# Kernel tuning notes

Measured on AMD Instinct MI355X. Metric: run time of the kernel, lower is better.

The kernel has to match this reference:

```python
import jax, jax.numpy as jnp
import numpy as np

B, N, D, S, ITERS = 64, 4096, 256, 8, 3
EPS = 1e-5


def _ln(x, g, b):
    m = jnp.mean(x, axis=-1, keepdims=True)
    v = jnp.mean((x - m) ** 2, axis=-1, keepdims=True)
    return (x - m) * jax.lax.rsqrt(v + EPS) * g + b


def setup_inputs() -> dict:
    key = jax.random.key(0)
    ks = jax.random.split(key, 20)
    s = 1.0 / np.sqrt(D)
    inp = {
        'x': jax.random.normal(ks[0], (B, N, D), jnp.float32),
        'noise': jax.random.normal(ks[1], (B, S, D), jnp.float32),
        'slot_mu': jax.random.normal(ks[2], (1, 1, D), jnp.float32),
        'slot_sigma': jax.random.normal(ks[3], (1, 1, D), jnp.float32) * 0.1,
        'Wq': jax.random.uniform(ks[4], (D, D), jnp.float32, -s, s),
        'bq': jnp.zeros((D,), jnp.float32),
        'Wk': jax.random.uniform(ks[5], (D, D), jnp.float32, -s, s),
        'bk': jnp.zeros((D,), jnp.float32),
        'Wv': jax.random.uniform(ks[6], (D, D), jnp.float32, -s, s),
        'bv': jnp.zeros((D,), jnp.float32),
        'W_ih': jax.random.uniform(ks[7], (3 * D, D), jnp.float32, -s, s),
        'b_ih': jnp.zeros((3 * D,), jnp.float32),
        'W_hh': jax.random.uniform(ks[8], (3 * D, D), jnp.float32, -s, s),
        'b_hh': jnp.zeros((3 * D,), jnp.float32),
        'W1': jax.random.uniform(ks[9], (D, D), jnp.float32, -s, s),
        'b1': jnp.zeros((D,), jnp.float32),
        'W2': jax.random.uniform(ks[10], (D, D), jnp.float32, -s, s),
        'b2': jnp.zeros((D,), jnp.float32),
        'g_in': jnp.ones((D,), jnp.float32), 'be_in': jnp.zeros((D,), jnp.float32),
        'g_sl': jnp.ones((D,), jnp.float32), 'be_sl': jnp.zeros((D,), jnp.float32),
        'g_mlp': jnp.ones((D,), jnp.float32), 'be_mlp': jnp.zeros((D,), jnp.float32),
    }
    return inp


def reference(x, noise, slot_mu, slot_sigma, Wq, bq, Wk, bk, Wv, bv,
              W_ih, b_ih, W_hh, b_hh, W1, b1, W2, b2,
              g_in, be_in, g_sl, be_sl, g_mlp, be_mlp):
    # slot init: mu + exp(sigma) * noise, broadcast over (B, S, D)
    slots = slot_mu + jnp.exp(slot_sigma) * noise

    xn = _ln(x, g_in, be_in)
    k = jnp.einsum('bnd,ed->bne', xn, Wk) + bk
    v = jnp.einsum('bnd,ed->bne', xn, Wv) + bv

    for _ in range(ITERS):
        sn = _ln(slots, g_sl, be_sl)
        q = jnp.einsum('bsd,ed->bse', sn, Wq) + bq
        attn_logits = jnp.einsum('bsd,bnd->bsn', q, k)
        attn = jax.nn.softmax(attn_logits, axis=-1)  # softmax over inputs N (as in source)
        updates = jnp.einsum('bnd,bsn->bsd', v, attn)

        # GRUCell: input=updates, hidden=slots (flattened over B*S)
        u = updates.reshape(-1, D)
        h = slots.reshape(-1, D)
        gx = u @ W_ih.T + b_ih
        gh = h @ W_hh.T + b_hh
        xr, xz, xn_g = jnp.split(gx, 3, axis=-1)
        hr, hz, hn_g = jnp.split(gh, 3, axis=-1)
        r = jax.nn.sigmoid(xr + hr)
        z = jax.nn.sigmoid(xz + hz)
        n = jnp.tanh(xn_g + r * hn_g)
        h = (1.0 - z) * n + z * h
        slots = h.reshape(x.shape[0], -1, D)

        m = _ln(slots, g_mlp, be_mlp)
        slots = slots + jax.nn.relu(m @ W1.T + b1) @ W2.T + b2
    return slots
```

## Files before the change

kernel.cpp:

```cpp
#include <hip/hip_runtime.h>

#define B_ 64
#define N_ 4096
#define D_ 256
#define S_ 8
#define EPSL 1e-5f

typedef _Float16 f16x8 __attribute__((ext_vector_type(8)));
typedef _Float16 f16x4 __attribute__((ext_vector_type(4)));
typedef float f32x4 __attribute__((ext_vector_type(4)));

__device__ __forceinline__ void gload_lds16(const void* g, void* l){
    __builtin_amdgcn_global_load_lds(
        (const __attribute__((address_space(1))) unsigned int*)g,
        (__attribute__((address_space(3))) unsigned int*)l, 16, 0, 0);
}

__global__ __launch_bounds__(256) void k_ln_x(const float* __restrict__ x,
        const float* __restrict__ g, const float* __restrict__ be,
        _Float16* __restrict__ xn) {
    int w = threadIdx.x >> 6, l = threadIdx.x & 63;
    long row = (long)blockIdx.x * 4 + w;
    float4 xv = *(const float4*)(x + row * D_ + l * 4);
    float s = xv.x + xv.y + xv.z + xv.w;
    float q = xv.x*xv.x + xv.y*xv.y + xv.z*xv.z + xv.w*xv.w;
    #pragma unroll
    for (int m = 1; m < 64; m <<= 1) { s += __shfl_xor(s, m); q += __shfl_xor(q, m); }
    float mean = s * (1.0f/D_);
    float var = q * (1.0f/D_) - mean*mean;
    float inv = rsqrtf(var + EPSL);
    float4 gv = *(const float4*)(g + l*4);
    float4 bv = *(const float4*)(be + l*4);
    f16x4 o;
    o[0] = (_Float16)((xv.x-mean)*inv*gv.x + bv.x);
    o[1] = (_Float16)((xv.y-mean)*inv*gv.y + bv.y);
    o[2] = (_Float16)((xv.z-mean)*inv*gv.z + bv.z);
    o[3] = (_Float16)((xv.w-mean)*inv*gv.w + bv.w);
    *(f16x4*)(xn + row * D_ + l*4) = o;
}

__global__ __launch_bounds__(256) void k_wprep(const float* __restrict__ Whh,
        const float* __restrict__ W1, const float* __restrict__ W2,
        _Float16* __restrict__ Whhf, _Float16* __restrict__ W1f,
        _Float16* __restrict__ W2f) {
    int r = blockIdx.x, t = threadIdx.x;
    const float* src; _Float16* dst; int row;
    if (r < 768){ src = Whh; dst = Whhf; row = r; }
    else if (r < 1024){ src = W1; dst = W1f; row = r - 768; }
    else { src = W2; dst = W2f; row = r - 1024; }
    float v = src[(long)(r < 768 ? r : (r < 1024 ? r-768 : r-1024))*256 + t];
    long di = (long)((((row>>4)*8 + (t>>5))*64 + ((t>>3)&3)*16 + (row&15)))*8 + (t&7);
    dst[di] = (_Float16)v;
}

__global__ __launch_bounds__(256) void k_wprep2(const float* __restrict__ Wih,
        const float* __restrict__ Wv, const float* __restrict__ Wq,
        const float* __restrict__ Wk, const float* __restrict__ bih,
        const float* __restrict__ bv, const float* __restrict__ bq,
        _Float16* __restrict__ Wcf, _Float16* __restrict__ Wqkf,
        float* __restrict__ bc, float* __restrict__ cq) {
    __shared__ float a[4][256];
    int r = blockIdx.x, t = threadIdx.x;
    int w = t>>6, l = t&63;
    bool isC = (r < 192);
    if (isC){
        #pragma unroll
        for (int k=0;k<4;k++) a[k][t] = Wih[(long)(r*4+k)*256 + t];
    } else {
        int dbase = (r-192)*4;
        #pragma unroll
        for (int k=0;k<4;k++) a[k][t] = Wk[(long)t*256 + dbase + k];
    }
    __syncthreads();
    float ac[4] = {0.f,0.f,0.f,0.f};
    const float* Bm = isC ? Wv : Wq;
    for (int e=0;e<256;e++){
        float bvv = Bm[(long)e*256 + t];
        ac[0] += a[0][e]*bvv; ac[1] += a[1][e]*bvv;
        ac[2] += a[2][e]*bvv; ac[3] += a[3][e]*bvv;
    }
    _Float16* dst = isC ? Wcf : Wqkf;
    int rb = isC ? r*4 : (r-192)*4;
    #pragma unroll
    for (int k=0;k<4;k++){
        int row = rb + k;
        long di = (long)((((row>>4)*8 + (t>>5))*64 + ((t>>3)&3)*16 + (row&15)))*8 + (t&7);
        dst[di] = (_Float16)ac[k];
    }
    if (w < 4){
        const float* bvec = isC ? bv : bq;
        float p = 0.f;
        #pragma unroll
        for (int q=0;q<4;q++) p += a[w][l + q*64] * bvec[l + q*64];
        #pragma unroll
        for (int m=1;m<64;m<<=1) p += __shfl_xor(p, m);
        if (l==0){
            if (isC) bc[r*4 + w] = p + bih[r*4 + w];
            else     cq[(r-192)*4 + w] = p;
        }
    }
}

__device__ __forceinline__ void a16_st4(_Float16* a, int row, int col, float4 v){
    int byte = row*512 + ((col*2) ^ ((row&7)<<4));
    f16x4 h; h[0]=(_Float16)v.x; h[1]=(_Float16)v.y; h[2]=(_Float16)v.z; h[3]=(_Float16)v.w;
    *(f16x4*)((char*)a + byte) = h;
}
__device__ __forceinline__ void a16_st2(_Float16* a, int row, int col, _Float16 v){
    int byte = row*512 + ((col*2) ^ ((row&7)<<4));
    *(_Float16*)((char*)a + byte) = v;
}
__device__ __forceinline__ f16x8 a16_ld8(const _Float16* a, int row, int col){
    int byte = row*512 + ((col*2) ^ ((row&7)<<4));
    return *(const f16x8*)((const char*)a + byte);
}
__device__ __forceinline__ f16x8 wfrag_ld(const _Float16* __restrict__ Wf,
        int tt, int ks, int l){
    return *(const f16x8*)(Wf + ((long)tt*4096 + (ks*64 + l)*8));
}

template<int NT, int OS>
__device__ __forceinline__ void mm_stage_f(const _Float16* a16,
        const _Float16* __restrict__ Wf, float* outl, int w, int l){
    int lr = l&15, lh = l>>4;
    f16x8 A[8];
    #pragma unroll
    for (int ks=0;ks<8;ks++) A[ks] = a16_ld8(a16, lr, lh*8 + ks*32);
    #pragma unroll
    for (int tile=0; tile<NT; ++tile){
        int tt = w*NT + tile;
        f32x4 acc = {0.f,0.f,0.f,0.f};
        #pragma unroll
        for (int ks=0;ks<8;ks++)
            acc = __builtin_amdgcn_mfma_f32_16x16x32_f16(A[ks], wfrag_ld(Wf,tt,ks,l), acc, 0,0,0);
        if (lh < 2){
            #pragma unroll
            for (int r=0;r<4;r++) outl[(lh*4+r)*OS + tt*16 + lr] = acc[r];
        }
    }
}

__device__ __forceinline__ void mm_gates_f(const _Float16* au, const _Float16* ah,
        const _Float16* __restrict__ Wcf, const _Float16* __restrict__ Whf,
        float* g1, float* g2, int w, int l){
    int lr = l&15, lh = l>>4;
    f16x8 Au[8], Ah[8];
    #pragma unroll
    for (int ks=0;ks<8;ks++){ Au[ks] = a16_ld8(au, lr, lh*8+ks*32);
                              Ah[ks] = a16_ld8(ah, lr, lh*8+ks*32); }
    #pragma unroll
    for (int tile=0; tile<6; ++tile){
        int tt = w*6 + tile;
        f32x4 a1 = {0.f,0.f,0.f,0.f}, a2 = {0.f,0.f,0.f,0.f};
        #pragma unroll
        for (int ks=0;ks<8;ks++)
            a1 = __builtin_amdgcn_mfma_f32_16x16x32_f16(Au[ks], wfrag_ld(Wcf,tt,ks,l), a1, 0,0,0);
        #pragma unroll
        for (int ks=0;ks<8;ks++)
            a2 = __builtin_amdgcn_mfma_f32_16x16x32_f16(Ah[ks], wfrag_ld(Whf,tt,ks,l), a2, 0,0,0);
        if (lh < 2){
            #pragma unroll
            for (int r=0;r<4;r++){
                int s = lh*4+r;
                g1[s*768 + tt*16 + lr] = a1[r];
                g2[s*768 + tt*16 + lr] = a2[r];
            }
        }
    }
}

__global__ __launch_bounds__(512) void k_init(const float* __restrict__ noise,
        const float* __restrict__ mu, const float* __restrict__ sg,
        const float* __restrict__ g_sl, const float* __restrict__ be_sl,
        const _Float16* __restrict__ Wqkf, const float* __restrict__ cq,
        float* __restrict__ slots, _Float16* __restrict__ qh16) {
    __shared__ __align__(16) _Float16 a16[16*256];
    __shared__ float g1[8*256];
    int t = threadIdx.x, w = t>>6, l = t&63, b = blockIdx.x;
    int col = l*4;
    float4 nz = *(const float4*)(noise + ((long)b*8+w)*256 + col);
    float4 muv = *(const float4*)(mu + col);
    float4 sgv = *(const float4*)(sg + col);
    float4 sl;
    sl.x = muv.x + __expf(sgv.x)*nz.x; sl.y = muv.y + __expf(sgv.y)*nz.y;
    sl.z = muv.z + __expf(sgv.z)*nz.z; sl.w = muv.w + __expf(sgv.w)*nz.w;
    *(float4*)(slots + ((long)b*8+w)*256 + col) = sl;
    float s1 = sl.x+sl.y+sl.z+sl.w;
    float s2 = sl.x*sl.x+sl.y*sl.y+sl.z*sl.z+sl.w*sl.w;
    #pragma unroll
    for (int m=1;m<64;m<<=1){ s1+=__shfl_xor(s1,m); s2+=__shfl_xor(s2,m); }
    float mean = s1*(1.0f/D_);
    float inv = rsqrtf(s2*(1.0f/D_) - mean*mean + EPSL);
    float4 gv = *(const float4*)(g_sl + col);
    float4 bb = *(const float4*)(be_sl + col);
    float4 sn;
    sn.x=(sl.x-mean)*inv*gv.x+bb.x; sn.y=(sl.y-mean)*inv*gv.y+bb.y;
    sn.z=(sl.z-mean)*inv*gv.z+bb.z; sn.w=(sl.w-mean)*inv*gv.w+bb.w;
    a16_st4(a16, w, col, sn);
    float4 z = {0.f,0.f,0.f,0.f};
    a16_st4(a16, 8+w, col, z);
    __syncthreads();
    mm_stage_f<2,256>(a16, Wqkf, g1, w, l);
    __syncthreads();
    for (int idx=t; idx<2048; idx+=512){
        int s = idx>>8, d = idx&255;
        qh16[((long)b*16+s)*D_ + d] = (_Float16)(g1[s*256+d] + cq[d]);
        qh16[((long)b*16+8+s)*D_ + d] = (_Float16)0.f;
    }
}

__global__ __launch_bounds__(256) void k_attn(const _Float16* __restrict__ xn,
        const _Float16* __restrict__ qh16,
        float* __restrict__ pacc, float* __restrict__ ppsum,
        float* __restrict__ pmax) {
    __shared__ __align__(16) char xt_raw[4*16384];
    __shared__ __align__(16) float pt_s[4][16][8];
    __shared__ float mw_s[4][8], psw_s[4][8];
    int t = threadIdx.x, w = t>>6, l = t&63, lr = l&15, lh = l>>4;
    int c = blockIdx.x, b = blockIdx.y;

    f16x8 A[8];
    const _Float16* qbase = qh16 + ((long)b*16 + lr)*D_ + lh*8;
    #pragma unroll
    for (int ks=0;ks<8;ks++) A[ks] = *(const f16x8*)(qbase + ks*32);
    asm volatile("s_waitcnt vmcnt(0)" ::: "memory");

    char* xw = xt_raw + w*16384;
    const char* xnb = (const char*)(xn + (long)b*N_*D_);
    int rlo = l>>5;
    int cb  = (l&31)*16;

    {
        int n0 = c*512 + w*16;
        #pragma unroll
        for (int j=0;j<8;j++){
            int row = 2*j + rlo;
            const char* gp = xnb + (long)(n0+row)*512 + (cb ^ ((row&7)<<4));
            gload_lds16(gp, xw + j*1024);
        }
    }

    float m8[8];
    #pragma unroll
    for (int s=0;s<8;s++) m8[s] = -1e30f;
    float acc[8][4] = {};
    float psr[4] = {0.f,0.f,0.f,0.f};
    float (*pt)[8] = pt_s[w];
    int fx = (lr&7)<<4;

    for (int sc=0; sc<8; ++sc){
        const char* curb = xw + ((sc&1)<<13);
        char* nxtb = xw + (((sc+1)&1)<<13);
        if (sc < 7){
            asm volatile("s_waitcnt lgkmcnt(0)" ::: "memory");
            int n0n = c*512 + (sc+1)*64 + w*16;
            #pragma unroll
            for (int j=0;j<8;j++){
                int row = 2*j + rlo;
                const char* gp = xnb + (long)(n0n+row)*512 + (cb ^ ((row&7)<<4));
                gload_lds16(gp, nxtb + j*1024);
            }
            asm volatile("s_waitcnt vmcnt(8)" ::: "memory");
        } else {
            asm volatile("s_waitcnt vmcnt(0)" ::: "memory");
        }
        __builtin_amdgcn_sched_barrier(0);

        f32x4 lacc = {0.f,0.f,0.f,0.f};
        #pragma unroll
        for (int ks=0;ks<8;ks++){
            f16x8 Bf = *(const f16x8*)(curb + lr*512 + ((lh*16 + ks*64) ^ fx));
            lacc = __builtin_amdgcn_mfma_f32_16x16x32_f16(A[ks], Bf, lacc, 0,0,0);
        }
        float tm[4];
        #pragma unroll
        for (int r=0;r<4;r++) tm[r] = lacc[r];
        #pragma unroll
        for (int m=1;m<16;m<<=1){
            #pragma unroll
            for (int r=0;r<4;r++) tm[r] = fmaxf(tm[r], __shfl_xor(tm[r], m));
        }
        float mN[8];
        #pragma unroll
        for (int r=0;r<4;r++){ mN[r] = __shfl(tm[r], lr); mN[4+r] = __shfl(tm[r], 16+lr); }
        float sc8[8];
        #pragma unroll
        for (int s=0;s<8;s++){
            float mn = fmaxf(m8[s], mN[s]);
            sc8[s] = __expf(m8[s] - mn);
            m8[s] = mn;
        }
        #pragma unroll
        for (int s=0;s<8;s++){
            acc[s][0]*=sc8[s]; acc[s][1]*=sc8[s]; acc[s][2]*=sc8[s]; acc[s][3]*=sc8[s];
        }
        if (lh < 2){
            float4 pv;
            #pragma unroll
            for (int r=0;r<4;r++){
                int s = lh*4+r;
                float p = __expf(lacc[r] - m8[s]);
                psr[r] = psr[r]*sc8[s] + p;
                ((float*)&pv)[r] = p;
            }
            *(float4*)&pt[lr][lh*4] = pv;
        }
        #pragma unroll 4
        for (int i=0;i<16;i++){
            float4 p0 = *(const float4*)&pt[i][0];
            float4 p1 = *(const float4*)&pt[i][4];
            f16x4 xv = *(const f16x4*)(curb + i*512 + ((l*8) ^ ((i&7)<<4)));
            float x0=(float)xv[0], x1=(float)xv[1], x2=(float)xv[2], x3=(float)xv[3];
            acc[0][0]+=p0.x*x0; acc[0][1]+=p0.x*x1; acc[0][2]+=p0.x*x2; acc[0][3]+=p0.x*x3;
            acc[1][0]+=p0.y*x0; acc[1][1]+=p0.y*x1; acc[1][2]+=p0.y*x2; acc[1][3]+=p0.y*x3;
            acc[2][0]+=p0.z*x0; acc[2][1]+=p0.z*x1; acc[2][2]+=p0.z*x2; acc[2][3]+=p0.z*x3;
            acc[3][0]+=p0.w*x0; acc[3][1]+=p0.w*x1; acc[3][2]+=p0.w*x2; acc[3][3]+=p0.w*x3;
            acc[4][0]+=p1.x*x0; acc[4][1]+=p1.x*x1; acc[4][2]+=p1.x*x2; acc[4][3]+=p1.x*x3;
            acc[5][0]+=p1.y*x0; acc[5][1]+=p1.y*x1; acc[5][2]+=p1.y*x2; acc[5][3]+=p1.y*x3;
            acc[6][0]+=p1.z*x0; acc[6][1]+=p1.z*x1; acc[6][2]+=p1.z*x2; acc[6][3]+=p1.z*x3;
            acc[7][0]+=p1.w*x0; acc[7][1]+=p1.w*x1; acc[7][2]+=p1.w*x2; acc[7][3]+=p1.w*x3;
        }
    }
    #pragma unroll
    for (int m=1;m<16;m<<=1){
        #pragma unroll
        for (int r=0;r<4;r++) psr[r] += __shfl_xor(psr[r], m);
    }
    if (l == 0){
        #pragma unroll
        for (int s=0;s<8;s++) mw_s[w][s] = m8[s];
        #pragma unroll
        for (int r=0;r<4;r++) psw_s[w][r] = psr[r];
    }
    if (l == 16){
        #pragma unroll
        for (int r=0;r<4;r++) psw_s[w][4+r] = psr[r];
    }
    __syncthreads();
    float M8[8];
    #pragma unroll
    for (int s=0;s<8;s++)
        M8[s] = fmaxf(fmaxf(mw_s[0][s],mw_s[1][s]), fmaxf(mw_s[2][s],mw_s[3][s]));
    float* accw = (float*)xt_raw;
    #pragma unroll
    for (int s=0;s<8;s++){
        float wsc = __expf(m8[s] - M8[s]);
        float4 v;
        v.x=acc[s][0]*wsc; v.y=acc[s][1]*wsc; v.z=acc[s][2]*wsc; v.w=acc[s][3]*wsc;
        *(float4*)&accw[((w*8+s)<<8) + l*4] = v;
    }
    __syncthreads();
    for (int pair=t; pair<2048; pair+=256){
        int s = pair>>8, d = pair&255;
        float v = accw[(s<<8)+d] + accw[((8+s)<<8)+d] + accw[((16+s)<<8)+d] + accw[((24+s)<<8)+d];
        pacc[(((long)b*8 + c)*8 + s)*D_ + d] = v;
    }
    if (t < 8){
        float ps = 0.f;
        #pragma unroll
        for (int w2=0;w2<4;w2++) ps += __expf(mw_s[w2][t]-M8[t]) * psw_s[w2][t];
        ppsum[((long)b*8+c)*8 + t] = ps;
        pmax [((long)b*8+c)*8 + t] = M8[t];
    }
}

__global__ __launch_bounds__(512) void k_tail(
    const float* __restrict__ pacc, const float* __restrict__ ppsum,
    const float* __restrict__ pmax, const float* __restrict__ slots,
    const _Float16* __restrict__ Wcf, const float* __restrict__ bc,
    const _Float16* __restrict__ Whhf, const float* __restrict__ bhh,
    const _Float16* __restrict__ W1f, const float* __restrict__ b1,
    const _Float16* __restrict__ W2f, const float* __restrict__ b2,
    const float* __restrict__ gm, const float* __restrict__ bem,
    const float* __restrict__ g_sl, const float* __restrict__ be_sl,
    const _Float16* __restrict__ Wqkf, const float* __restrict__ cq,
    float* __restrict__ out, _Float16* __restrict__ qh16, int last) {
    int t = threadIdx.x, w = t>>6, l = t&63;
    int b = blockIdx.x;
    __shared__ float hb[8][256], hn[8][256];
    __shared__ float g1[8*768], g2[8*768];
    __shared__ __align__(16) _Float16 a16a[16*256], a16b[16*256];
    __shared__ float pss[8];
    __shared__ float wcs[8][8];

    if (t < 8){
        float pm[8]; float M = -1e30f;
        #pragma unroll
        for (int c=0;c<8;c++){ pm[c] = pmax[((long)b*8+c)*8+t]; M = fmaxf(M, pm[c]); }
        float ps = 0.f;
        #pragma unroll
        for (int c=0;c<8;c++){
            float wc = __expf(pm[c]-M);
            wcs[t][c] = wc;
            ps += wc*ppsum[((long)b*8+c)*8+t];
        }
        pss[t] = ps;
    }
    __syncthreads();
    for (int idx=t; idx<2048; idx+=512){
        int s = idx>>8, d = idx&255;
        float v = 0.f;
        #pragma unroll
        for (int c=0;c<8;c++) v += wcs[s][c]*pacc[(((long)b*8+c)*8+s)*D_ + d];
        float axv = v / pss[s];
        float hbv = slots[((long)b*8+s)*D_ + d];
        hb[s][d] = hbv;
        a16_st2(a16a, s, d, (_Float16)axv);
        a16_st2(a16b, s, d, (_Float16)hbv);
    }
    {   float4 z = {0.f,0.f,0.f,0.f};
        a16_st4(a16a, 8+w, l*4, z);
        a16_st4(a16b, 8+w, l*4, z);
    }
    __syncthreads();
    mm_gates_f(a16a, a16b, Wcf, Whhf, g1, g2, w, l);
    __syncthreads();
    {
        int d0 = l*4;
        float hn4[4];
        #pragma unroll
        for (int i=0;i<4;i++){
            int d = d0+i;
            float r = 1.f/(1.f+__expf(-(g1[w*768+d]     + bc[d]     + g2[w*768+d]     + bhh[d])));
            float z = 1.f/(1.f+__expf(-(g1[w*768+256+d] + bc[256+d] + g2[w*768+256+d] + bhh[256+d])));
            float gg = g1[w*768+512+d] + bc[512+d] + r*(g2[w*768+512+d] + bhh[512+d]);
            float e2 = __expf(2.f*gg);
            float nn = 1.f - 2.f/(e2+1.f);
            hn4[i] = (1.f-z)*nn + z*hb[w][d];
            hn[w][d] = hn4[i];
        }
        float s1 = hn4[0]+hn4[1]+hn4[2]+hn4[3];
        float s2 = hn4[0]*hn4[0]+hn4[1]*hn4[1]+hn4[2]*hn4[2]+hn4[3]*hn4[3];
        #pragma unroll
        for (int m=1;m<64;m<<=1){ s1+=__shfl_xor(s1,m); s2+=__shfl_xor(s2,m); }
        float mean = s1*(1.0f/D_);
        float inv = rsqrtf(s2*(1.0f/D_) - mean*mean + EPSL);
        float4 gv = *(const float4*)(gm + d0);
        float4 bb = *(const float4*)(bem + d0);
        float4 v;
        v.x=(hn4[0]-mean)*inv*gv.x+bb.x; v.y=(hn4[1]-mean)*inv*gv.y+bb.y;
        v.z=(hn4[2]-mean)*inv*gv.z+bb.z; v.w=(hn4[3]-mean)*inv*gv.w+bb.w;
        a16_st4(a16a, w, d0, v);
    }
    __syncthreads();
    mm_stage_f<2,256>(a16a, W1f, g1, w, l);
    __syncthreads();
    {
        int d0 = l*4;
        float4 v = *(const float4*)&g1[w*256+d0];
        float4 bb = *(const float4*)(b1 + d0);
        v.x=fmaxf(v.x+bb.x,0.f); v.y=fmaxf(v.y+bb.y,0.f);
        v.z=fmaxf(v.z+bb.z,0.f); v.w=fmaxf(v.w+bb.w,0.f);
        a16_st4(a16b, w, d0, v);
    }
    __syncthreads();
    mm_stage_f<2,256>(a16b, W2f, g2, w, l);
    __syncthreads();
    {
        int d0 = l*4;
        float4 bb = *(const float4*)(b2 + d0);
        float4 o4;
        o4.x = hn[w][d0]   + g2[w*256+d0]   + bb.x;
        o4.y = hn[w][d0+1] + g2[w*256+d0+1] + bb.y;
        o4.z = hn[w][d0+2] + g2[w*256+d0+2] + bb.z;
        o4.w = hn[w][d0+3] + g2[w*256+d0+3] + bb.w;
        *(float4*)(out + ((long)b*8+w)*D_ + d0) = o4;
        if (!last){
            float s1 = o4.x+o4.y+o4.z+o4.w;
            float s2 = o4.x*o4.x+o4.y*o4.y+o4.z*o4.z+o4.w*o4.w;
            #pragma unroll
            for (int m=1;m<64;m<<=1){ s1+=__shfl_xor(s1,m); s2+=__shfl_xor(s2,m); }
            float mean = s1*(1.0f/D_);
            float inv = rsqrtf(s2*(1.0f/D_) - mean*mean + EPSL);
            float4 gv = *(const float4*)(g_sl + d0);
            float4 be = *(const float4*)(be_sl + d0);
            float4 v;
            v.x=(o4.x-mean)*inv*gv.x+be.x; v.y=(o4.y-mean)*inv*gv.y+be.y;
            v.z=(o4.z-mean)*inv*gv.z+be.z; v.w=(o4.w-mean)*inv*gv.w+be.w;
            a16_st4(a16a, w, d0, v);
        }
    }
    if (last) return;
    __syncthreads();
    mm_stage_f<2,256>(a16a, Wqkf, g1, w, l);
    __syncthreads();
    for (int idx=t; idx<2048; idx+=512){
        int s = idx>>8, d = idx&255;
        qh16[((long)b*16+s)*D_ + d] = (_Float16)(g1[s*256+d] + cq[d]);
    }
}

extern "C" void kernel_launch(void* const* d_in, const int* in_sizes, int n_in,
                              void* d_out, int out_size, void* d_ws, size_t ws_size,
                              hipStream_t stream) {
    const float* x     = (const float*)d_in[0];
    const float* noise = (const float*)d_in[1];
    const float* mu    = (const float*)d_in[2];
    const float* sg    = (const float*)d_in[3];
    const float* Wq    = (const float*)d_in[4];
    const float* bq    = (const float*)d_in[5];
    const float* Wk    = (const float*)d_in[6];
    const float* Wv    = (const float*)d_in[8];
    const float* bv    = (const float*)d_in[9];
    const float* Wih   = (const float*)d_in[10];
    const float* bih   = (const float*)d_in[11];
    const float* Whh   = (const float*)d_in[12];
    const float* bhh   = (const float*)d_in[13];
    const float* W1    = (const float*)d_in[14];
    const float* b1    = (const float*)d_in[15];
    const float* W2    = (const float*)d_in[16];
    const float* b2    = (const float*)d_in[17];
    const float* g_in  = (const float*)d_in[18];
    const float* be_in = (const float*)d_in[19];
    const float* g_sl  = (const float*)d_in[20];
    const float* be_sl = (const float*)d_in[21];
    const float* g_mlp = (const float*)d_in[22];
    const float* be_mlp= (const float*)d_in[23];

    char* ws = (char*)d_ws;
    _Float16* xn16  = (_Float16*)(ws);
    _Float16* qh16  = (_Float16*)(ws + 134217728);
    float*    slots = (float*)   (ws + 134742016);
    float*    pacc  = (float*)   (ws + 135266304);
    float*    ppsum = (float*)   (ws + 152043520);
    float*    pmax  = (float*)   (ws + 152059904);
    _Float16* w16f  = (_Float16*)(ws + 152076288);
    float*    bc    = (float*)   (ws + 153255936);
    float*    cq    = (float*)   (ws + 153259008);

    _Float16* Wcf  = w16f;
    _Float16* Whhf = w16f + 196608;
    _Float16* W1f  = w16f + 393216;
    _Float16* W2f  = w16f + 458752;
    _Float16* Wqkf = w16f + 524288;

    hipLaunchKernelGGL(k_wprep, dim3(1280), dim3(256), 0, stream,
                       Whh, W1, W2, Whhf, W1f, W2f);
    hipLaunchKernelGGL(k_wprep2, dim3(256), dim3(256), 0, stream,
                       Wih, Wv, Wq, Wk, bih, bv, bq, Wcf, Wqkf, bc, cq);
    hipLaunchKernelGGL(k_ln_x, dim3(65536), dim3(256), 0, stream, x, g_in, be_in, xn16);
    hipLaunchKernelGGL(k_init, dim3(64), dim3(512), 0, stream,
                       noise, mu, sg, g_sl, be_sl, Wqkf, cq, slots, qh16);
    for (int it = 0; it < 3; it++){
        hipLaunchKernelGGL(k_attn, dim3(8,64), dim3(256), 0, stream,
                           xn16, qh16, pacc, ppsum, pmax);
        float* dst = (it==2) ? (float*)d_out : slots;
        hipLaunchKernelGGL(k_tail, dim3(64), dim3(512), 0, stream,
                           pacc, ppsum, pmax, slots,
                           Wcf, bc, Whhf, bhh, W1f, b1, W2f, b2,
                           g_mlp, be_mlp, g_sl, be_sl, Wqkf, cq,
                           dst, qh16, (it==2) ? 1 : 0);
    }
}
```

Measured before the change: 273.6 us.

## Move attention P·V accumulation to MFMA with transposed LDS reads and lazy rescale

Replaces the scalar FMA loop that accumulates softmax-weighted values in the attention kernel with 16x16x16 f16 MFMAs. Probabilities are stored to LDS as f16, and both operands are loaded with ds_read_b64_tr_b16 transposed reads. The LDS tile layout drops the XOR swizzle in favour of a layout suited to the transposed reads. The online-softmax rescale is deferred unless the running max grows by more than a threshold. This adds f16 rounding of the probabilities, which lowers precision, and a possible LDS bank-conflict change from removing the swizzle.

```diff
diff --git a/kernel.cpp b/kernel.cpp
--- a/kernel.cpp
+++ b/kernel.cpp
@@ -14,6 +14,16 @@
     __builtin_amdgcn_global_load_lds(
         (const __attribute__((address_space(1))) unsigned int*)g,
         (__attribute__((address_space(3))) unsigned int*)l, 16, 0, 0);
+}
+
+__device__ __forceinline__ unsigned lds_off(const void* p){
+    return (unsigned)(size_t)(const __attribute__((address_space(3))) char*)p;
+}
+
+__device__ __forceinline__ f16x4 tr16(unsigned off){
+    f16x4 d;
+    asm volatile("ds_read_b64_tr_b16 %0, %1" : "=v"(d) : "v"(off));
+    return d;
 }
 
 __global__ __launch_bounds__(256) void k_ln_x(const float* __restrict__ x,
@@ -214,7 +224,8 @@
         float* __restrict__ pacc, float* __restrict__ ppsum,
         float* __restrict__ pmax) {
     __shared__ __align__(16) char xt_raw[4*16384];
-    __shared__ __align__(16) float pt_s[4][16][8];
+    __shared__ __align__(16) char pt16_s[4][512];
+    __shared__ __align__(16) float scl_s[4][16];
     __shared__ float mw_s[4][8], psw_s[4][8];
     int t = threadIdx.x, w = t>>6, l = t&63, lr = l&15, lh = l>>4;
     int c = blockIdx.x, b = blockIdx.y;
@@ -226,40 +237,47 @@
     asm volatile("s_waitcnt vmcnt(0)" ::: "memory");
 
     char* xw = xt_raw + w*16384;
+    char* pt16w = pt16_s[w];
+    float* sclw = scl_s[w];
     const char* xnb = (const char*)(xn + (long)b*N_*D_);
-    int rlo = l>>5;
-    int cb  = (l&31)*16;
+
+    if (l < 16) sclw[l] = 1.f;
+    if (l < 32){
+        long long z = 0;
+        *(long long*)(pt16w + (l>>1)*32 + 16 + (l&1)*8) = z;
+    }
+
+    int P0 = ((l>>1)&15)*512 + (l>>5)*32 + (l&1)*16;
 
     {
         int n0 = c*512 + w*16;
-        #pragma unroll
-        for (int j=0;j<8;j++){
-            int row = 2*j + rlo;
-            const char* gp = xnb + (long)(n0+row)*512 + (cb ^ ((row&7)<<4));
-            gload_lds16(gp, xw + j*1024);
-        }
+        const char* gp0 = xnb + (long)n0*512 + P0;
+        #pragma unroll
+        for (int j=0;j<8;j++) gload_lds16(gp0 + j*64, xw + j*1024);
     }
 
     float m8[8];
     #pragma unroll
     for (int s=0;s<8;s++) m8[s] = -1e30f;
-    float acc[8][4] = {};
+    f32x4 acc4[16];
+    #pragma unroll
+    for (int dt=0;dt<16;dt++) acc4[dt] = (f32x4){0.f,0.f,0.f,0.f};
     float psr[4] = {0.f,0.f,0.f,0.f};
-    float (*pt)[8] = pt_s[w];
-    int fx = (lr&7)<<4;
+
+    int lbo = lr*32 + (lh>>1)*512 + (lh&1)*16;
+    unsigned pt_off = lds_off(pt16w) + l*8;
+    int lhbit = lh & 1;
 
     for (int sc=0; sc<8; ++sc){
         const char* curb = xw + ((sc&1)<<13);
         char* nxtb = xw + (((sc+1)&1)<<13);
+        unsigned cur_off = lds_off(curb) + l*8;
         if (sc < 7){
             asm volatile("s_waitcnt lgkmcnt(0)" ::: "memory");
             int n0n = c*512 + (sc+1)*64 + w*16;
-            #pragma unroll
-            for (int j=0;j<8;j++){
-                int row = 2*j + rlo;
-                const char* gp = xnb + (long)(n0n+row)*512 + (cb ^ ((row&7)<<4));
-                gload_lds16(gp, nxtb + j*1024);
-            }
+            const char* gp = xnb + (long)n0n*512 + P0;
+            #pragma unroll
+            for (int j=0;j<8;j++) gload_lds16(gp + j*64, nxtb + j*1024);
             asm volatile("s_waitcnt vmcnt(8)" ::: "memory");
         } else {
             asm volatile("s_waitcnt vmcnt(0)" ::: "memory");
@@ -269,7 +287,7 @@
         f32x4 lacc = {0.f,0.f,0.f,0.f};
         #pragma unroll
         for (int ks=0;ks<8;ks++){
-            f16x8 Bf = *(const f16x8*)(curb + lr*512 + ((lh*16 + ks*64) ^ fx));
+            f16x8 Bf = *(const f16x8*)(curb + ks*1024 + lbo);
             lacc = __builtin_amdgcn_mfma_f32_16x16x32_f16(A[ks], Bf, lacc, 0,0,0);
         }
         float tm[4];
@@ -283,43 +301,51 @@
         float mN[8];
         #pragma unroll
         for (int r=0;r<4;r++){ mN[r] = __shfl(tm[r], lr); mN[4+r] = __shfl(tm[r], 16+lr); }
-        float sc8[8];
-        #pragma unroll
-        for (int s=0;s<8;s++){
-            float mn = fmaxf(m8[s], mN[s]);
-            sc8[s] = __expf(m8[s] - mn);
-            m8[s] = mn;
-        }
-        #pragma unroll
-        for (int s=0;s<8;s++){
-            acc[s][0]*=sc8[s]; acc[s][1]*=sc8[s]; acc[s][2]*=sc8[s]; acc[s][3]*=sc8[s];
+        float gmx = mN[0]-m8[0];
+        #pragma unroll
+        for (int s=1;s<8;s++) gmx = fmaxf(gmx, mN[s]-m8[s]);
+        if (gmx > 8.f){
+            float sc8[8];
+            #pragma unroll
+            for (int s=0;s<8;s++){
+                float mn2 = fmaxf(m8[s], mN[s]);
+                sc8[s] = __expf(m8[s]-mn2);
+                m8[s] = mn2;
+            }
+            if (l == 0){
+                #pragma unroll
+                for (int s=0;s<8;s++) sclw[s] = sc8[s];
+            }
+            asm volatile("s_waitcnt lgkmcnt(0)" ::: "memory");
+            __builtin_amdgcn_sched_barrier(0);
+            f32x4 s4 = *(const f32x4*)&sclw[(l>>4)*4];
+            #pragma unroll
+            for (int dt=0;dt<16;dt++) acc4[dt] *= s4;
+            #pragma unroll
+            for (int r=0;r<4;r++) psr[r] *= (lhbit ? sc8[4+r] : sc8[r]);
         }
         if (lh < 2){
-            float4 pv;
+            f16x4 pv;
             #pragma unroll
             for (int r=0;r<4;r++){
-                int s = lh*4+r;
-                float p = __expf(lacc[r] - m8[s]);
-                psr[r] = psr[r]*sc8[s] + p;
-                ((float*)&pv)[r] = p;
+                float m8s = lhbit ? m8[4+r] : m8[r];
+                float p = __expf(lacc[r] - m8s);
+                psr[r] += p;
+                pv[r] = (_Float16)p;
             }
-            *(float4*)&pt[lr][lh*4] = pv;
-        }
-        #pragma unroll 4
-        for (int i=0;i<16;i++){
-            float4 p0 = *(const float4*)&pt[i][0];
-            float4 p1 = *(const float4*)&pt[i][4];
-            f16x4 xv = *(const f16x4*)(curb + i*512 + ((l*8) ^ ((i&7)<<4)));
-            float x0=(float)xv[0], x1=(float)xv[1], x2=(float)xv[2], x3=(float)xv[3];
-            acc[0][0]+=p0.x*x0; acc[0][1]+=p0.x*x1; acc[0][2]+=p0.x*x2; acc[0][3]+=p0.x*x3;
-            acc[1][0]+=p0.y*x0; acc[1][1]+=p0.y*x1; acc[1][2]+=p0.y*x2; acc[1][3]+=p0.y*x3;
-            acc[2][0]+=p0.z*x0; acc[2][1]+=p0.z*x1; acc[2][2]+=p0.z*x2; acc[2][3]+=p0.z*x3;
-            acc[3][0]+=p0.w*x0; acc[3][1]+=p0.w*x1; acc[3][2]+=p0.w*x2; acc[3][3]+=p0.w*x3;
-            acc[4][0]+=p1.x*x0; acc[4][1]+=p1.x*x1; acc[4][2]+=p1.x*x2; acc[4][3]+=p1.x*x3;
-            acc[5][0]+=p1.y*x0; acc[5][1]+=p1.y*x1; acc[5][2]+=p1.y*x2; acc[5][3]+=p1.y*x3;
-            acc[6][0]+=p1.z*x0; acc[6][1]+=p1.z*x1; acc[6][2]+=p1.z*x2; acc[6][3]+=p1.z*x3;
-            acc[7][0]+=p1.w*x0; acc[7][1]+=p1.w*x1; acc[7][2]+=p1.w*x2; acc[7][3]+=p1.w*x3;
-        }
+            *(f16x4*)(pt16w + lr*32 + lh*8) = pv;
+        }
+        asm volatile("s_waitcnt lgkmcnt(0)" ::: "memory");
+        __builtin_amdgcn_sched_barrier(0);
+        f16x4 pa = tr16(pt_off);
+        f16x4 bt[16];
+        #pragma unroll
+        for (int dt=0;dt<16;dt++) bt[dt] = tr16(cur_off + dt*512);
+        asm volatile("s_waitcnt lgkmcnt(0)" ::: "memory");
+        __builtin_amdgcn_sched_barrier(0);
+        #pragma unroll
+        for (int dt=0;dt<16;dt++)
+            acc4[dt] = __builtin_amdgcn_mfma_f32_16x16x16f16(pa, bt[dt], acc4[dt], 0,0,0);
     }
     #pragma unroll
     for (int m=1;m<16;m<<=1){
@@ -342,12 +368,18 @@
     for (int s=0;s<8;s++)
         M8[s] = fmaxf(fmaxf(mw_s[0][s],mw_s[1][s]), fmaxf(mw_s[2][s],mw_s[3][s]));
     float* accw = (float*)xt_raw;
-    #pragma unroll
-    for (int s=0;s<8;s++){
-        float wsc = __expf(m8[s] - M8[s]);
-        float4 v;
-        v.x=acc[s][0]*wsc; v.y=acc[s][1]*wsc; v.z=acc[s][2]*wsc; v.w=acc[s][3]*wsc;
-        *(float4*)&accw[((w*8+s)<<8) + l*4] = v;
+    int sbase = l>>4;
+    if (sbase < 2){
+        #pragma unroll
+        for (int r=0;r<4;r++){
+            float m8s = lhbit ? m8[4+r] : m8[r];
+            float M8s = lhbit ? M8[4+r] : M8[r];
+            float wsc = __expf(m8s - M8s);
+            int s = sbase*4 + r;
+            #pragma unroll
+            for (int dt=0;dt<16;dt++)
+                accw[((w*8 + s)<<8) + dt*16 + lr] = acc4[dt][r]*wsc;
+        }
     }
     __syncthreads();
     for (int pair=t; pair<2048; pair+=256){
```

Result: slower. 284.4 us (+4.0%).
